# Kernel optimization log

Measured on AMD Instinct MI355X. Metric: run time of the kernel, lower is better.

Reference implementation:

```python
import jax, jax.numpy as jnp
import numpy as np

B, L, DC, DD, A = 32, 1024, 1024, 1024, 1024
NEG = -1e10


def setup_inputs() -> dict:
    key = jax.random.key(0)
    ks = jax.random.split(key, 16)
    s = lambda fan_in: 1.0 / np.sqrt(fan_in)
    return {
        "caption_features": jax.random.normal(ks[0], (B, L, DC), jnp.float32),
        "decoder_hidden": jax.random.normal(ks[1], (B, DD), jnp.float32),
        "word": jax.random.normal(ks[2], (B, DC), jnp.float32),
        "prev_caption_mask": jax.random.randint(ks[3], (B, L), 0, 2, jnp.int32),
        # cap_features_att: Linear(DC, A)
        "Wf": jax.random.uniform(ks[4], (A, DC), jnp.float32, -s(DC), s(DC)),
        "bf": jax.random.uniform(ks[5], (A,), jnp.float32, -s(DC), s(DC)),
        # cap_decoder_att: Linear(DD, A)
        "Wd": jax.random.uniform(ks[6], (A, DD), jnp.float32, -s(DD), s(DD)),
        "bd": jax.random.uniform(ks[7], (A,), jnp.float32, -s(DD), s(DD)),
        # cap_full_att: Linear(A, 1)
        "Wa": jax.random.uniform(ks[8], (1, A), jnp.float32, -s(A), s(A)),
        "ba": jax.random.uniform(ks[9], (1,), jnp.float32, -s(A), s(A)),
        # context_gate: Linear(2*DC + DD, DC)
        "Wg": jax.random.uniform(ks[10], (DC, 2 * DC + DD), jnp.float32, -s(2 * DC + DD), s(2 * DC + DD)),
        "bg": jax.random.uniform(ks[11], (DC,), jnp.float32, -s(2 * DC + DD), s(2 * DC + DD)),
        # sc_affine: Linear(DC, DC)
        "Ws": jax.random.uniform(ks[12], (DC, DC), jnp.float32, -s(DC), s(DC)),
        "bs": jax.random.uniform(ks[13], (DC,), jnp.float32, -s(DC), s(DC)),
        # tc_affine: Linear(2*DD, DC)
        "Wt": jax.random.uniform(ks[14], (DC, 2 * DD), jnp.float32, -s(2 * DD), s(2 * DD)),
        "bt": jax.random.uniform(ks[15], (DC,), jnp.float32, -s(2 * DD), s(2 * DD)),
    }


def reference(caption_features, decoder_hidden, word, prev_caption_mask,
              Wf, bf, Wd, bd, Wa, ba, Wg, bg, Ws, bs, Wt, bt):
    # additive (Bahdanau) attention scores: (B, L)
    att1 = jnp.einsum('bld,ad->bla', caption_features, Wf) + bf          # (B, L, A)
    att2 = decoder_hidden @ Wd.T + bd                                    # (B, A)
    scores = jnp.einsum('bla,a->bl', jnp.tanh(att1 + att2[:, None, :]), Wa[0]) + ba[0]
    scores = jnp.where(prev_caption_mask == 0, NEG, scores)
    alpha = jax.nn.softmax(scores, axis=1)                               # (B, L)
    context = jnp.einsum('bl,bld->bd', alpha, caption_features)          # (B, DC)
    # gated fusion
    zt = jax.nn.sigmoid(jnp.concatenate([word, decoder_hidden, context], axis=1) @ Wg.T + bg)
    sc = jnp.tanh(context @ Ws.T + bs)
    tc = jnp.tanh(jnp.concatenate([word, decoder_hidden], axis=1) @ Wt.T + bt)
    gated_context = zt * sc + (1.0 - zt) * tc
    return (gated_context, alpha)
```

## Files before the change

kernel.cpp:

```cpp
#include <hip/hip_runtime.h>
#include <hip/hip_bf16.h>
#include <cstdint>
#include <cstddef>

#define LOG2E 1.4426950408889634f

typedef __attribute__((ext_vector_type(8))) short short8;
typedef __attribute__((ext_vector_type(4))) float f32x4;

__device__ __forceinline__ float exp2f_fast(float x) { return __builtin_amdgcn_exp2f(x); }
__device__ __forceinline__ float rcp_fast(float x)   { return __builtin_amdgcn_rcpf(x); }
__device__ __forceinline__ float tanh_fast(float x) {
  float e = exp2f_fast(x * (2.0f * LOG2E));
  return 1.0f - 2.0f * rcp_fast(e + 1.0f);
}
__device__ __forceinline__ unsigned short f2b(float f) {
  union { float f; unsigned int u; } v; v.f = f;
  return (unsigned short)((v.u + 0x7FFFu + ((v.u >> 16) & 1u)) >> 16);
}
__device__ __forceinline__ float b2f(short h) {
  union { unsigned u; float f; } w; w.u = ((unsigned)(unsigned short)h) << 16;
  return w.f;
}

#define GLOAD_LDS16(g, l) \
  __builtin_amdgcn_global_load_lds((const __attribute__((address_space(1))) unsigned int*)(g), \
                                   (__attribute__((address_space(3))) unsigned int*)(l), 16, 0, 0)

__device__ __forceinline__ void skinny_gemm(
    const float* __restrict__ W, int Kfull,
    const float* __restrict__ x0, const float* __restrict__ x1,
    const float* __restrict__ x2,
    int kbeg, int kend, int n0, float* __restrict__ out)
{
  __shared__ unsigned char sX[4096];
  const int tid = threadIdx.x, lane = tid & 63, wv = tid >> 6;
  const int l15 = lane & 15, l4 = lane >> 4;
  f32x4 acc[2][2];
#pragma unroll
  for (int m = 0; m < 2; ++m)
#pragma unroll
    for (int j = 0; j < 2; ++j) acc[m][j] = (f32x4){0.f, 0.f, 0.f, 0.f};

  const int srow = tid >> 3, skc = (tid & 7) * 8;
  const int sbyte = srow * 128 + ((skc * 2) ^ ((srow & 7) << 4));

  for (int k0 = kbeg; k0 < kend; k0 += 64) {
    const float* xs = (k0 < 1024) ? x0 : (k0 < 2048) ? x1 : x2;
    const float* xp = xs + srow * 1024 + (k0 & 1023) + skc;
    float4 a = *reinterpret_cast<const float4*>(xp);
    float4 b = *reinterpret_cast<const float4*>(xp + 4);
    short8 h;
    h[0] = (short)f2b(a.x); h[1] = (short)f2b(a.y); h[2] = (short)f2b(a.z); h[3] = (short)f2b(a.w);
    h[4] = (short)f2b(b.x); h[5] = (short)f2b(b.y); h[6] = (short)f2b(b.z); h[7] = (short)f2b(b.w);
    *reinterpret_cast<short8*>(sX + sbyte) = h;
    __syncthreads();
#pragma unroll
    for (int ks = 0; ks < 2; ++ks) {
      short8 af[2], bfr[2];
#pragma unroll
      for (int m = 0; m < 2; ++m) {
        int r = m * 16 + l15;
        af[m] = *reinterpret_cast<const short8*>(
            sX + r * 128 + (((ks * 64) + l4 * 16) ^ ((r & 7) << 4)));
      }
#pragma unroll
      for (int j = 0; j < 2; ++j) {
        int n = n0 + wv * 32 + j * 16 + l15;
        const float* wp = W + (size_t)n * Kfull + k0 + ks * 32 + l4 * 8;
        float4 wa = *reinterpret_cast<const float4*>(wp);
        float4 wb = *reinterpret_cast<const float4*>(wp + 4);
        short8 hb;
        hb[0] = (short)f2b(wa.x); hb[1] = (short)f2b(wa.y); hb[2] = (short)f2b(wa.z); hb[3] = (short)f2b(wa.w);
        hb[4] = (short)f2b(wb.x); hb[5] = (short)f2b(wb.y); hb[6] = (short)f2b(wb.z); hb[7] = (short)f2b(wb.w);
        bfr[j] = hb;
      }
#pragma unroll
      for (int m = 0; m < 2; ++m)
#pragma unroll
        for (int j = 0; j < 2; ++j)
          acc[m][j] = __builtin_amdgcn_mfma_f32_16x16x32_bf16(af[m], bfr[j], acc[m][j], 0, 0, 0);
    }
    __syncthreads();
  }
#pragma unroll
  for (int m = 0; m < 2; ++m)
#pragma unroll
    for (int j = 0; j < 2; ++j)
#pragma unroll
      for (int r = 0; r < 4; ++r)
        atomicAdd(out + (size_t)(m * 16 + l4 * 4 + r) * 1024 + (n0 + wv * 32 + j * 16 + l15),
                  acc[m][j][r]);
}

__global__ __launch_bounds__(256) void convert_att2(
    const float* __restrict__ cap, const float* __restrict__ wf,
    unsigned short* __restrict__ capb, unsigned short* __restrict__ wfb,
    const float* __restrict__ Wd, const float* __restrict__ dh,
    float* __restrict__ att2, int nconv)
{
  if ((int)blockIdx.x < nconv) {
    const int NC = 33554432 / 8;
    const int NT = NC + 1048576 / 8;
    for (int c = blockIdx.x * 256 + threadIdx.x; c < NT; c += nconv * 256) {
      const float* s; unsigned short* d; int off;
      if (c < NC) { s = cap; d = capb; off = c * 8; }
      else        { s = wf;  d = wfb;  off = (c - NC) * 8; }
      float4 a = *reinterpret_cast<const float4*>(s + off);
      float4 b = *reinterpret_cast<const float4*>(s + off + 4);
      short8 o;
      o[0] = (short)f2b(a.x); o[1] = (short)f2b(a.y); o[2] = (short)f2b(a.z); o[3] = (short)f2b(a.w);
      o[4] = (short)f2b(b.x); o[5] = (short)f2b(b.y); o[6] = (short)f2b(b.z); o[7] = (short)f2b(b.w);
      *reinterpret_cast<short8*>(d + off) = o;
    }
  } else {
    int bid2 = blockIdx.x - nconv;
    int nt = bid2 & 7, ks = bid2 >> 3;
    skinny_gemm(Wd, 1024, dh, dh, dh, ks * 512, ks * 512 + 512, nt * 128, att2);
  }
}

__global__ __launch_bounds__(256) void gate_gemm(
    const float* __restrict__ Wg, const float* __restrict__ Ws_,
    const float* __restrict__ Wt, const float* __restrict__ word,
    const float* __restrict__ dh, const float* __restrict__ ctx,
    float* __restrict__ ztp, float* __restrict__ scp, float* __restrict__ tcp)
{
  const int nt = blockIdx.x, slot = blockIdx.y;
  if (slot < 6)
    skinny_gemm(Wg, 3072, word, dh, ctx, slot * 512, slot * 512 + 512, nt * 128, ztp);
  else if (slot < 8)
    skinny_gemm(Ws_, 1024, ctx, ctx, ctx, (slot - 6) * 512, (slot - 6) * 512 + 512, nt * 128, scp);
  else
    skinny_gemm(Wt, 2048, word, dh, dh, (slot - 8) * 512, (slot - 8) * 512 + 512, nt * 128, tcp);
}

__global__ __launch_bounds__(512, 2) void att_gemm3(
    const unsigned short* __restrict__ capb, const unsigned short* __restrict__ wfb,
    const float* __restrict__ att2pre, const float* __restrict__ bfv,
    const float* __restrict__ bdv, const float* __restrict__ Wa,
    float* __restrict__ scores)
{
  __shared__ __align__(16) unsigned char lds[131072];
  const int tid = threadIdx.x, lane = tid & 63, wv = tid >> 6;
  const int j = ((int)blockIdx.x & 7) * 64 + ((int)blockIdx.x >> 3);
  const int mt = j >> 2, nt = j & 3;
  const int m0 = mt << 8, n0 = nt << 8;
  const int bb = m0 >> 10;
  const int wm = wv >> 2, wn = wv & 3;
  const int l15 = lane & 15, l4 = lane >> 4;
  const int r8 = lane >> 3, c8 = lane & 7;
  const unsigned swb = (unsigned)((l15 & 7) << 4);

  const unsigned char* aSrc = (const unsigned char*)capb +
      (size_t)(m0 + wv * 32 + r8) * 2048 + ((c8 * 16) ^ (r8 << 4));
  const unsigned char* bSrc = (const unsigned char*)wfb +
      (size_t)(n0 + wv * 32 + r8) * 2048 + ((c8 * 16) ^ (r8 << 4));
  const unsigned ldsBase = (unsigned)(size_t)(&lds[0]);

  f32x4 acc[8][4];
#pragma unroll
  for (int mf = 0; mf < 8; ++mf)
#pragma unroll
    for (int nf = 0; nf < 4; ++nf) acc[mf][nf] = (f32x4){0.f, 0.f, 0.f, 0.f};

#define STAGE(t) do { \
    const int sl__ = (t) & 1; \
    unsigned char* da__ = lds + sl__ * 65536 + wv * 4096; \
    unsigned char* db__ = lds + sl__ * 65536 + 32768 + wv * 4096; \
    const unsigned char* ga__ = aSrc + (t) * 128; \
    const unsigned char* gb__ = bSrc + (t) * 128; \
    GLOAD_LDS16(ga__,          da__); \
    GLOAD_LDS16(ga__ + 16384,  da__ + 1024); \
    GLOAD_LDS16(ga__ + 32768,  da__ + 2048); \
    GLOAD_LDS16(ga__ + 49152,  da__ + 3072); \
    GLOAD_LDS16(gb__,          db__); \
    GLOAD_LDS16(gb__ + 16384,  db__ + 1024); \
    GLOAD_LDS16(gb__ + 32768,  db__ + 2048); \
    GLOAD_LDS16(gb__ + 49152,  db__ + 3072); \
  } while (0)

#define DSREAD(dst, addr) \
  asm volatile("ds_read_b128 %0, %1" : "=v"(dst) : "v"(addr))

#define READ_AQ(dst, q) do { \
_Pragma("unroll") \
    for (int mf2 = 0; mf2 < 2; ++mf2) \
_Pragma("unroll") \
      for (int ks = 0; ks < 2; ++ks) { \
        unsigned r__ = (unsigned)(wm * 128 + (q) * 32 + mf2 * 16 + l15); \
        DSREAD(dst[mf2 * 2 + ks], sA + r__ * 128 + (((unsigned)(ks * 64 + l4 * 16)) ^ swb)); \
      } \
  } while (0)

#define READ_B(ch) do { \
_Pragma("unroll") \
    for (int nf = 0; nf < 2; ++nf) \
_Pragma("unroll") \
      for (int ks = 0; ks < 2; ++ks) { \
        unsigned c__ = (unsigned)(wn * 64 + (ch) * 32 + nf * 16 + l15); \
        DSREAD(Breg[(ch) * 4 + nf * 2 + ks], sB + c__ * 128 + (((unsigned)(ks * 64 + l4 * 16)) ^ swb)); \
      } \
  } while (0)

#define MFMA8(q, ch, Aq) do { \
    __builtin_amdgcn_s_setprio(1); \
_Pragma("unroll") \
    for (int mf2 = 0; mf2 < 2; ++mf2) \
_Pragma("unroll") \
      for (int nf = 0; nf < 2; ++nf) \
_Pragma("unroll") \
        for (int ks = 0; ks < 2; ++ks) \
          acc[(q) * 2 + mf2][(ch) * 2 + nf] = __builtin_amdgcn_mfma_f32_16x16x32_bf16( \
              Aq[mf2 * 2 + ks], Breg[(ch) * 4 + nf * 2 + ks], acc[(q) * 2 + mf2][(ch) * 2 + nf], 0, 0, 0); \
    __builtin_amdgcn_s_setprio(0); \
  } while (0)

#define WAIT_LGKM(n) do { \
    asm volatile("s_waitcnt lgkmcnt(" #n ")" ::: "memory"); \
    __builtin_amdgcn_sched_barrier(0); \
  } while (0)

  short8 Aq0[4], Aq1[4], Breg[8];

  STAGE(0);
  asm volatile("s_waitcnt vmcnt(0)" ::: "memory");
  asm volatile("s_barrier" ::: "memory");

  for (int t = 0; t < 16; ++t) {
    const unsigned sA = ldsBase + (unsigned)((t & 1) * 65536);
    const unsigned sB = sA + 32768u;

    if (t < 15) STAGE(t + 1);

    READ_AQ(Aq0, 0);
    READ_B(0);
    READ_B(1);
    READ_AQ(Aq1, 1);

    WAIT_LGKM(8);
    MFMA8(0, 0, Aq0);
    WAIT_LGKM(4);
    MFMA8(0, 1, Aq0);
    WAIT_LGKM(0);
    READ_AQ(Aq0, 2);
    MFMA8(1, 0, Aq1);
    MFMA8(1, 1, Aq1);
    READ_AQ(Aq1, 3);
    WAIT_LGKM(4);
    MFMA8(2, 0, Aq0);
    MFMA8(2, 1, Aq0);
    WAIT_LGKM(0);
    MFMA8(3, 0, Aq1);
    MFMA8(3, 1, Aq1);

    if (t < 15) {
      asm volatile("s_waitcnt vmcnt(0)" ::: "memory");
      asm volatile("s_barrier" ::: "memory");
    }
  }

  float colb[4], wav[4];
#pragma unroll
  for (int nf = 0; nf < 4; ++nf) {
    int cg = n0 + wn * 64 + nf * 16 + l15;
    colb[nf] = att2pre[bb * 1024 + cg] + bfv[cg] + bdv[cg];
    wav[nf]  = Wa[cg];
  }
#pragma unroll
  for (int mf = 0; mf < 8; ++mf) {
#pragma unroll
    for (int r = 0; r < 4; ++r) {
      float s = tanh_fast(acc[mf][0][r] + colb[0]) * wav[0]
              + tanh_fast(acc[mf][1][r] + colb[1]) * wav[1]
              + tanh_fast(acc[mf][2][r] + colb[2]) * wav[2]
              + tanh_fast(acc[mf][3][r] + colb[3]) * wav[3];
      s += __shfl_xor(s, 1);
      s += __shfl_xor(s, 2);
      s += __shfl_xor(s, 4);
      s += __shfl_xor(s, 8);
      if (l15 == 0)
        atomicAdd(scores + (m0 + wm * 128 + mf * 16 + l4 * 4 + r), s);
    }
  }
#undef STAGE
#undef DSREAD
#undef READ_AQ
#undef READ_B
#undef MFMA8
#undef WAIT_LGKM
}

__global__ __launch_bounds__(256) void softmax_k(
    const float* __restrict__ scores, const int* __restrict__ mask,
    float* __restrict__ alpha)
{
  const int b = blockIdx.x, tid = threadIdx.x;
  __shared__ float red[8];
  float s[4];
  float mx = -3.0e38f;
#pragma unroll
  for (int i = 0; i < 4; ++i) {
    int l = tid + i * 256;
    float v = scores[b * 1024 + l];
    v = (mask[b * 1024 + l] == 0) ? -1.0e10f : v;
    s[i] = v;
    mx = fmaxf(mx, v);
  }
  for (int off = 1; off < 64; off <<= 1) mx = fmaxf(mx, __shfl_xor(mx, off));
  int wv = tid >> 6;
  if ((tid & 63) == 0) red[wv] = mx;
  __syncthreads();
  mx = fmaxf(fmaxf(red[0], red[1]), fmaxf(red[2], red[3]));
  float sum = 0.f;
#pragma unroll
  for (int i = 0; i < 4; ++i) {
    s[i] = exp2f_fast((s[i] - mx) * LOG2E);
    sum += s[i];
  }
  for (int off = 1; off < 64; off <<= 1) sum += __shfl_xor(sum, off);
  if ((tid & 63) == 0) red[4 + wv] = sum;
  __syncthreads();
  sum = red[4] + red[5] + red[6] + red[7];
  float inv = 1.0f / sum;
#pragma unroll
  for (int i = 0; i < 4; ++i) alpha[b * 1024 + tid + i * 256] = s[i] * inv;
}

__global__ __launch_bounds__(256) void ctx_kb(
    const unsigned short* __restrict__ capb, const float* __restrict__ alpha,
    float* __restrict__ ctx)
{
  const int b = blockIdx.y, lc = blockIdx.x;
  const int dc = threadIdx.x & 127, loff = threadIdx.x >> 7;
  float acc[8] = {0.f, 0.f, 0.f, 0.f, 0.f, 0.f, 0.f, 0.f};
  for (int l = lc * 128 + loff; l < lc * 128 + 128; l += 2) {
    float av = alpha[b * 1024 + l];
    if (av != 0.f) {
      short8 v = *reinterpret_cast<const short8*>(capb + (((size_t)(b * 1024 + l)) << 10) + dc * 8);
#pragma unroll
      for (int j = 0; j < 8; ++j) acc[j] += av * b2f(v[j]);
    }
  }
#pragma unroll
  for (int j = 0; j < 8; ++j) atomicAdd(ctx + b * 1024 + dc * 8 + j, acc[j]);
}

__global__ __launch_bounds__(256) void final_k(
    const float* __restrict__ ztp, const float* __restrict__ scp,
    const float* __restrict__ tcp, const float* __restrict__ bg,
    const float* __restrict__ bs, const float* __restrict__ bt,
    float* __restrict__ out)
{
  const int idx = blockIdx.x * 256 + threadIdx.x;
  const int d = idx & 1023;
  float z  = rcp_fast(1.0f + exp2f_fast(-(ztp[idx] + bg[d]) * LOG2E));
  float sc = tanh_fast(scp[idx] + bs[d]);
  float tc = tanh_fast(tcp[idx] + bt[d]);
  out[idx] = z * sc + (1.0f - z) * tc;
}

extern "C" void kernel_launch(void* const* d_in, const int* in_sizes, int n_in,
                              void* d_out, int out_size, void* d_ws, size_t ws_size,
                              hipStream_t stream) {
  const float* cap  = (const float*)d_in[0];
  const float* dh   = (const float*)d_in[1];
  const float* word = (const float*)d_in[2];
  const int*   mask = (const int*)d_in[3];
  const float* Wf   = (const float*)d_in[4];
  const float* bf   = (const float*)d_in[5];
  const float* Wd   = (const float*)d_in[6];
  const float* bd   = (const float*)d_in[7];
  const float* Wa   = (const float*)d_in[8];
  const float* Wg   = (const float*)d_in[10];
  const float* bg   = (const float*)d_in[11];
  const float* Ws   = (const float*)d_in[12];
  const float* bs   = (const float*)d_in[13];
  const float* Wt   = (const float*)d_in[14];
  const float* bt   = (const float*)d_in[15];

  float* out_g = (float*)d_out;
  float* alpha = (float*)d_out + 32768;

  float* att2pre = (float*)d_ws;
  float* scores  = att2pre + 32768;
  float* ctx     = scores + 32768;
  float* ztp     = ctx + 32768;
  float* scp     = ztp + 32768;
  float* tcp     = scp + 32768;
  unsigned short* capb = (unsigned short*)((char*)d_ws + 786432);
  unsigned short* wfb  = capb + 33554432;

  hipMemsetAsync(d_ws, 0, 6 * 32768 * sizeof(float), stream);

  convert_att2<<<2064, 256, 0, stream>>>(cap, Wf, capb, wfb, Wd, dh, att2pre, 2048);
  att_gemm3<<<512, 512, 0, stream>>>(capb, wfb, att2pre, bf, bd, Wa, scores);
  softmax_k<<<32, 256, 0, stream>>>(scores, mask, alpha);
  ctx_kb<<<dim3(8, 32), 256, 0, stream>>>(capb, alpha, ctx);
  gate_gemm<<<dim3(8, 12), 256, 0, stream>>>(Wg, Ws, Wt, word, dh, ctx, ztp, scp, tcp);
  final_k<<<128, 256, 0, stream>>>(ztp, scp, tcp, bg, bs, bt, out_g);
}
```

Measured before the change: 170.9 us.

## Skip bf16 conversion of masked caption rows and load Wf fragments directly from global

The conversion kernel now uses one block per fixed chunk and checks the caption mask. It skips the fp32-to-bf16 conversion of rows whose mask is zero, which cuts HBM read and write traffic roughly in proportion to the masked fraction. The attention GEMM no longer stages the Wf tile through LDS: B fragments are loaded straight from global memory into registers, halving LDS use and removing half of the ds_reads. The risk is that masked rows of capb keep stale or uninitialized workspace contents. If those contents contain NaN or Inf bit patterns, they can reach the context sum through 0*NaN, and the direct global B loads may raise GEMM memory latency.

```diff
diff --git a/kernel.cpp b/kernel.cpp
--- a/kernel.cpp
+++ b/kernel.cpp
@@ -97,24 +97,40 @@
     const float* __restrict__ cap, const float* __restrict__ wf,
     unsigned short* __restrict__ capb, unsigned short* __restrict__ wfb,
     const float* __restrict__ Wd, const float* __restrict__ dh,
-    float* __restrict__ att2, int nconv)
-{
-  if ((int)blockIdx.x < nconv) {
-    const int NC = 33554432 / 8;
-    const int NT = NC + 1048576 / 8;
-    for (int c = blockIdx.x * 256 + threadIdx.x; c < NT; c += nconv * 256) {
-      const float* s; unsigned short* d; int off;
-      if (c < NC) { s = cap; d = capb; off = c * 8; }
-      else        { s = wf;  d = wfb;  off = (c - NC) * 8; }
-      float4 a = *reinterpret_cast<const float4*>(s + off);
-      float4 b = *reinterpret_cast<const float4*>(s + off + 4);
+    float* __restrict__ att2, const int* __restrict__ mask)
+{
+  const int bid = blockIdx.x;
+  if (bid < 4096) {
+    const int base = bid * 1024;
+#pragma unroll
+    for (int j = 0; j < 4; ++j) {
+      int g = base + j * 256 + (int)threadIdx.x;
+      int row = g >> 7;
+      if (mask[row] != 0) {
+        const float* s = cap + (size_t)g * 8;
+        float4 a = *reinterpret_cast<const float4*>(s);
+        float4 b = *reinterpret_cast<const float4*>(s + 4);
+        short8 o;
+        o[0] = (short)f2b(a.x); o[1] = (short)f2b(a.y); o[2] = (short)f2b(a.z); o[3] = (short)f2b(a.w);
+        o[4] = (short)f2b(b.x); o[5] = (short)f2b(b.y); o[6] = (short)f2b(b.z); o[7] = (short)f2b(b.w);
+        *reinterpret_cast<short8*>(capb + (size_t)g * 8) = o;
+      }
+    }
+  } else if (bid < 4224) {
+    const int base = (bid - 4096) * 1024;
+#pragma unroll
+    for (int j = 0; j < 4; ++j) {
+      int g = base + j * 256 + (int)threadIdx.x;
+      const float* s = wf + (size_t)g * 8;
+      float4 a = *reinterpret_cast<const float4*>(s);
+      float4 b = *reinterpret_cast<const float4*>(s + 4);
       short8 o;
       o[0] = (short)f2b(a.x); o[1] = (short)f2b(a.y); o[2] = (short)f2b(a.z); o[3] = (short)f2b(a.w);
       o[4] = (short)f2b(b.x); o[5] = (short)f2b(b.y); o[6] = (short)f2b(b.z); o[7] = (short)f2b(b.w);
-      *reinterpret_cast<short8*>(d + off) = o;
+      *reinterpret_cast<short8*>(wfb + (size_t)g * 8) = o;
     }
   } else {
-    int bid2 = blockIdx.x - nconv;
+    int bid2 = bid - 4224;
     int nt = bid2 & 7, ks = bid2 >> 3;
     skinny_gemm(Wd, 1024, dh, dh, dh, ks * 512, ks * 512 + 512, nt * 128, att2);
   }
@@ -141,7 +157,7 @@
     const float* __restrict__ bdv, const float* __restrict__ Wa,
     float* __restrict__ scores)
 {
-  __shared__ __align__(16) unsigned char lds[131072];
+  __shared__ __align__(16) unsigned char lds[65536];
   const int tid = threadIdx.x, lane = tid & 63, wv = tid >> 6;
   const int j = ((int)blockIdx.x & 7) * 64 + ((int)blockIdx.x >> 3);
   const int mt = j >> 2, nt = j & 3;
@@ -154,8 +170,7 @@
 
   const unsigned char* aSrc = (const unsigned char*)capb +
       (size_t)(m0 + wv * 32 + r8) * 2048 + ((c8 * 16) ^ (r8 << 4));
-  const unsigned char* bSrc = (const unsigned char*)wfb +
-      (size_t)(n0 + wv * 32 + r8) * 2048 + ((c8 * 16) ^ (r8 << 4));
+  const unsigned short* bPtr = wfb + (size_t)(n0 + wn * 64 + l15) * 1024 + l4 * 8;
   const unsigned ldsBase = (unsigned)(size_t)(&lds[0]);
 
   f32x4 acc[8][4];
@@ -166,18 +181,12 @@
 
 #define STAGE(t) do { \
     const int sl__ = (t) & 1; \
-    unsigned char* da__ = lds + sl__ * 65536 + wv * 4096; \
-    unsigned char* db__ = lds + sl__ * 65536 + 32768 + wv * 4096; \
+    unsigned char* da__ = lds + sl__ * 32768 + wv * 4096; \
     const unsigned char* ga__ = aSrc + (t) * 128; \
-    const unsigned char* gb__ = bSrc + (t) * 128; \
     GLOAD_LDS16(ga__,          da__); \
     GLOAD_LDS16(ga__ + 16384,  da__ + 1024); \
     GLOAD_LDS16(ga__ + 32768,  da__ + 2048); \
     GLOAD_LDS16(ga__ + 49152,  da__ + 3072); \
-    GLOAD_LDS16(gb__,          db__); \
-    GLOAD_LDS16(gb__ + 16384,  db__ + 1024); \
-    GLOAD_LDS16(gb__ + 32768,  db__ + 2048); \
-    GLOAD_LDS16(gb__ + 49152,  db__ + 3072); \
   } while (0)
 
 #define DSREAD(dst, addr) \
@@ -193,14 +202,13 @@
       } \
   } while (0)
 
-#define READ_B(ch) do { \
+#define LOAD_B(ch, t) do { \
 _Pragma("unroll") \
     for (int nf = 0; nf < 2; ++nf) \
 _Pragma("unroll") \
-      for (int ks = 0; ks < 2; ++ks) { \
-        unsigned c__ = (unsigned)(wn * 64 + (ch) * 32 + nf * 16 + l15); \
-        DSREAD(Breg[(ch) * 4 + nf * 2 + ks], sB + c__ * 128 + (((unsigned)(ks * 64 + l4 * 16)) ^ swb)); \
-      } \
+      for (int ks = 0; ks < 2; ++ks) \
+        Breg[(ch) * 4 + nf * 2 + ks] = *reinterpret_cast<const short8*>( \
+            bPtr + (size_t)((ch) * 32 + nf * 16) * 1024 + (t) * 64 + ks * 32); \
   } while (0)
 
 #define MFMA8(q, ch, Aq) do { \
@@ -228,19 +236,17 @@
   asm volatile("s_barrier" ::: "memory");
 
   for (int t = 0; t < 16; ++t) {
-    const unsigned sA = ldsBase + (unsigned)((t & 1) * 65536);
-    const unsigned sB = sA + 32768u;
-
+    const unsigned sA = ldsBase + (unsigned)((t & 1) * 32768);
+
+    LOAD_B(0, t);
+    LOAD_B(1, t);
     if (t < 15) STAGE(t + 1);
 
     READ_AQ(Aq0, 0);
-    READ_B(0);
-    READ_B(1);
     READ_AQ(Aq1, 1);
 
-    WAIT_LGKM(8);
+    WAIT_LGKM(4);
     MFMA8(0, 0, Aq0);
-    WAIT_LGKM(4);
     MFMA8(0, 1, Aq0);
     WAIT_LGKM(0);
     READ_AQ(Aq0, 2);
@@ -286,7 +292,7 @@
 #undef STAGE
 #undef DSREAD
 #undef READ_AQ
-#undef READ_B
+#undef LOAD_B
 #undef MFMA8
 #undef WAIT_LGKM
 }
@@ -393,7 +399,7 @@
 
   hipMemsetAsync(d_ws, 0, 6 * 32768 * sizeof(float), stream);
 
-  convert_att2<<<2064, 256, 0, stream>>>(cap, Wf, capb, wfb, Wd, dh, att2pre, 2048);
+  convert_att2<<<4240, 256, 0, stream>>>(cap, Wf, capb, wfb, Wd, dh, att2pre, mask);
   att_gemm3<<<512, 512, 0, stream>>>(capb, wfb, att2pre, bf, bd, Wa, scores);
   softmax_k<<<32, 256, 0, stream>>>(scores, mask, alpha);
   ctx_kb<<<dim3(8, 32), 256, 0, stream>>>(capb, alpha, ctx);
```

Result: slower. 196.6 us (+15.0%).

## Fuse caption fp32-to-bf16 conversion into attention GEMM staging loop

Applied to the files above, without the earlier changes.

The separate pass that converted the whole 128MB fp32 caption tensor to bf16 in workspace is removed. The attention GEMM now loads fp32 caption tiles into registers, packs them to bf16 and writes them into LDS itself, while weight tiles still use direct global-to-LDS loads. The context kernel reads fp32 captions directly. This removes a full read and write of the large tensor, but the GEMM reads twice as many bytes per A tile, uses more registers and VALU work, and waits on the register prefetch.

```diff
diff --git a/kernel.cpp b/kernel.cpp
--- a/kernel.cpp
+++ b/kernel.cpp
@@ -94,27 +94,26 @@
 }
 
 __global__ __launch_bounds__(256) void convert_att2(
-    const float* __restrict__ cap, const float* __restrict__ wf,
-    unsigned short* __restrict__ capb, unsigned short* __restrict__ wfb,
+    const float* __restrict__ wf, unsigned short* __restrict__ wfb,
     const float* __restrict__ Wd, const float* __restrict__ dh,
-    float* __restrict__ att2, int nconv)
-{
-  if ((int)blockIdx.x < nconv) {
-    const int NC = 33554432 / 8;
-    const int NT = NC + 1048576 / 8;
-    for (int c = blockIdx.x * 256 + threadIdx.x; c < NT; c += nconv * 256) {
-      const float* s; unsigned short* d; int off;
-      if (c < NC) { s = cap; d = capb; off = c * 8; }
-      else        { s = wf;  d = wfb;  off = (c - NC) * 8; }
-      float4 a = *reinterpret_cast<const float4*>(s + off);
-      float4 b = *reinterpret_cast<const float4*>(s + off + 4);
+    float* __restrict__ att2)
+{
+  const int bid = blockIdx.x;
+  if (bid < 128) {
+    const int base = bid * 1024;
+#pragma unroll
+    for (int j = 0; j < 4; ++j) {
+      int g = base + j * 256 + (int)threadIdx.x;
+      const float* s = wf + (size_t)g * 8;
+      float4 a = *reinterpret_cast<const float4*>(s);
+      float4 b = *reinterpret_cast<const float4*>(s + 4);
       short8 o;
       o[0] = (short)f2b(a.x); o[1] = (short)f2b(a.y); o[2] = (short)f2b(a.z); o[3] = (short)f2b(a.w);
       o[4] = (short)f2b(b.x); o[5] = (short)f2b(b.y); o[6] = (short)f2b(b.z); o[7] = (short)f2b(b.w);
-      *reinterpret_cast<short8*>(d + off) = o;
+      *reinterpret_cast<short8*>(wfb + (size_t)g * 8) = o;
     }
   } else {
-    int bid2 = blockIdx.x - nconv;
+    int bid2 = bid - 128;
     int nt = bid2 & 7, ks = bid2 >> 3;
     skinny_gemm(Wd, 1024, dh, dh, dh, ks * 512, ks * 512 + 512, nt * 128, att2);
   }
@@ -136,7 +135,7 @@
 }
 
 __global__ __launch_bounds__(512, 2) void att_gemm3(
-    const unsigned short* __restrict__ capb, const unsigned short* __restrict__ wfb,
+    const float* __restrict__ cap, const unsigned short* __restrict__ wfb,
     const float* __restrict__ att2pre, const float* __restrict__ bfv,
     const float* __restrict__ bdv, const float* __restrict__ Wa,
     float* __restrict__ scores)
@@ -152,8 +151,8 @@
   const int r8 = lane >> 3, c8 = lane & 7;
   const unsigned swb = (unsigned)((l15 & 7) << 4);
 
-  const unsigned char* aSrc = (const unsigned char*)capb +
-      (size_t)(m0 + wv * 32 + r8) * 2048 + ((c8 * 16) ^ (r8 << 4));
+  const float* capA = cap + (size_t)(m0 + wv * 32 + r8) * 1024 +
+                      ((unsigned)((c8 * 16) ^ (r8 << 4)) >> 1);
   const unsigned char* bSrc = (const unsigned char*)wfb +
       (size_t)(n0 + wv * 32 + r8) * 2048 + ((c8 * 16) ^ (r8 << 4));
   const unsigned ldsBase = (unsigned)(size_t)(&lds[0]);
@@ -164,22 +163,34 @@
 #pragma unroll
     for (int nf = 0; nf < 4; ++nf) acc[mf][nf] = (f32x4){0.f, 0.f, 0.f, 0.f};
 
-#define STAGE(t) do { \
+#define STAGE_B(t) do { \
     const int sl__ = (t) & 1; \
-    unsigned char* da__ = lds + sl__ * 65536 + wv * 4096; \
     unsigned char* db__ = lds + sl__ * 65536 + 32768 + wv * 4096; \
-    const unsigned char* ga__ = aSrc + (t) * 128; \
     const unsigned char* gb__ = bSrc + (t) * 128; \
-    GLOAD_LDS16(ga__,          da__); \
-    GLOAD_LDS16(ga__ + 16384,  da__ + 1024); \
-    GLOAD_LDS16(ga__ + 32768,  da__ + 2048); \
-    GLOAD_LDS16(ga__ + 49152,  da__ + 3072); \
     GLOAD_LDS16(gb__,          db__); \
     GLOAD_LDS16(gb__ + 16384,  db__ + 1024); \
     GLOAD_LDS16(gb__ + 32768,  db__ + 2048); \
     GLOAD_LDS16(gb__ + 49152,  db__ + 3072); \
   } while (0)
 
+#define FLIGHT(fA0, fA1, fB0, fB1, j0, tt) do { \
+    const float* p0__ = capA + (size_t)(j0) * 8192 + (tt) * 64; \
+    const float* p1__ = p0__ + 8192; \
+    fA0 = *reinterpret_cast<const float4*>(p0__); \
+    fA1 = *reinterpret_cast<const float4*>(p0__ + 4); \
+    fB0 = *reinterpret_cast<const float4*>(p1__); \
+    fB1 = *reinterpret_cast<const float4*>(p1__ + 4); \
+  } while (0)
+
+#define PACK_WRITE(fA, fB, wp) do { \
+    short8 o__; \
+    o__[0] = (short)f2b(fA.x); o__[1] = (short)f2b(fA.y); \
+    o__[2] = (short)f2b(fA.z); o__[3] = (short)f2b(fA.w); \
+    o__[4] = (short)f2b(fB.x); o__[5] = (short)f2b(fB.y); \
+    o__[6] = (short)f2b(fB.z); o__[7] = (short)f2b(fB.w); \
+    *reinterpret_cast<short8*>(wp) = o__; \
+  } while (0)
+
 #define DSREAD(dst, addr) \
   asm volatile("ds_read_b128 %0, %1" : "=v"(dst) : "v"(addr))
 
@@ -222,16 +233,29 @@
   } while (0)
 
   short8 Aq0[4], Aq1[4], Breg[8];
-
-  STAGE(0);
+  float4 g0a, g0b, g1a, g1b;
+  float4 g2a, g2b, g3a, g3b;
+
+  STAGE_B(0);
+  FLIGHT(g0a, g0b, g1a, g1b, 0, 0);
+  FLIGHT(g2a, g2b, g3a, g3b, 2, 0);
   asm volatile("s_waitcnt vmcnt(0)" ::: "memory");
+  {
+    unsigned char* wp = lds + wv * 4096 + lane * 16;
+    PACK_WRITE(g0a, g0b, wp);
+    PACK_WRITE(g1a, g1b, wp + 1024);
+    PACK_WRITE(g2a, g2b, wp + 2048);
+    PACK_WRITE(g3a, g3b, wp + 3072);
+  }
+  WAIT_LGKM(0);
   asm volatile("s_barrier" ::: "memory");
 
   for (int t = 0; t < 16; ++t) {
     const unsigned sA = ldsBase + (unsigned)((t & 1) * 65536);
     const unsigned sB = sA + 32768u;
-
-    if (t < 15) STAGE(t + 1);
+    unsigned char* wp = lds + ((t + 1) & 1) * 65536 + wv * 4096 + lane * 16;
+
+    if (t < 15) STAGE_B(t + 1);
 
     READ_AQ(Aq0, 0);
     READ_B(0);
@@ -250,12 +274,21 @@
     WAIT_LGKM(4);
     MFMA8(2, 0, Aq0);
     MFMA8(2, 1, Aq0);
+    if (t < 15) FLIGHT(g0a, g0b, g1a, g1b, 0, t + 1);
     WAIT_LGKM(0);
     MFMA8(3, 0, Aq1);
     MFMA8(3, 1, Aq1);
-
     if (t < 15) {
+      FLIGHT(g2a, g2b, g3a, g3b, 2, t + 1);
+      asm volatile("s_waitcnt vmcnt(4)" ::: "memory");
+      __builtin_amdgcn_sched_barrier(0);
+      PACK_WRITE(g0a, g0b, wp);
+      PACK_WRITE(g1a, g1b, wp + 1024);
       asm volatile("s_waitcnt vmcnt(0)" ::: "memory");
+      __builtin_amdgcn_sched_barrier(0);
+      PACK_WRITE(g2a, g2b, wp + 2048);
+      PACK_WRITE(g3a, g3b, wp + 3072);
+      WAIT_LGKM(0);
       asm volatile("s_barrier" ::: "memory");
     }
   }
@@ -283,7 +316,9 @@
         atomicAdd(scores + (m0 + wm * 128 + mf * 16 + l4 * 4 + r), s);
     }
   }
-#undef STAGE
+#undef STAGE_B
+#undef FLIGHT
+#undef PACK_WRITE
 #undef DSREAD
 #undef READ_AQ
 #undef READ_B
@@ -328,7 +363,7 @@
 }
 
 __global__ __launch_bounds__(256) void ctx_kb(
-    const unsigned short* __restrict__ capb, const float* __restrict__ alpha,
+    const float* __restrict__ cap, const float* __restrict__ alpha,
     float* __restrict__ ctx)
 {
   const int b = blockIdx.y, lc = blockIdx.x;
@@ -337,9 +372,13 @@
   for (int l = lc * 128 + loff; l < lc * 128 + 128; l += 2) {
     float av = alpha[b * 1024 + l];
     if (av != 0.f) {
-      short8 v = *reinterpret_cast<const short8*>(capb + (((size_t)(b * 1024 + l)) << 10) + dc * 8);
-#pragma unroll
-      for (int j = 0; j < 8; ++j) acc[j] += av * b2f(v[j]);
+      const float* p = cap + (((size_t)(b * 1024 + l)) << 10) + dc * 8;
+      float4 v0 = *reinterpret_cast<const float4*>(p);
+      float4 v1 = *reinterpret_cast<const float4*>(p + 4);
+      acc[0] += av * v0.x; acc[1] += av * v0.y;
+      acc[2] += av * v0.z; acc[3] += av * v0.w;
+      acc[4] += av * v1.x; acc[5] += av * v1.y;
+      acc[6] += av * v1.z; acc[7] += av * v1.w;
     }
   }
 #pragma unroll
@@ -388,15 +427,14 @@
   float* ztp     = ctx + 32768;
   float* scp     = ztp + 32768;
   float* tcp     = scp + 32768;
-  unsigned short* capb = (unsigned short*)((char*)d_ws + 786432);
-  unsigned short* wfb  = capb + 33554432;
+  unsigned short* wfb = (unsigned short*)((char*)d_ws + 786432);
 
   hipMemsetAsync(d_ws, 0, 6 * 32768 * sizeof(float), stream);
 
-  convert_att2<<<2064, 256, 0, stream>>>(cap, Wf, capb, wfb, Wd, dh, att2pre, 2048);
-  att_gemm3<<<512, 512, 0, stream>>>(capb, wfb, att2pre, bf, bd, Wa, scores);
+  convert_att2<<<144, 256, 0, stream>>>(Wf, wfb, Wd, dh, att2pre);
+  att_gemm3<<<512, 512, 0, stream>>>(cap, wfb, att2pre, bf, bd, Wa, scores);
   softmax_k<<<32, 256, 0, stream>>>(scores, mask, alpha);
-  ctx_kb<<<dim3(8, 32), 256, 0, stream>>>(capb, alpha, ctx);
+  ctx_kb<<<dim3(8, 32), 256, 0, stream>>>(cap, alpha, ctx);
   gate_gemm<<<dim3(8, 12), 256, 0, stream>>>(Wg, Ws, Wt, word, dh, ctx, ztp, scp, tcp);
   final_k<<<128, 256, 0, stream>>>(ztp, scp, tcp, bg, bs, bt, out_g);
 }
```

Measured after the change: 162.7 us. 4.8% less time.
